# Kernel tuning notes

Measured on AMD Instinct MI355X. Metric: run time of the kernel, lower is better.

The kernel has to match this reference:

```python
import jax, jax.numpy as jnp
import numpy as np

BLOCK_SIZE = 256

def setup_inputs() -> dict:
    key = jax.random.key(0)
    k1, k2, k3 = jax.random.split(key, 3)
    B, H, S, D = 2, 16, 2048, 128
    return {
        "query": jax.random.normal(k1, (B, H, S, D), dtype=jnp.float32),
        "key": jax.random.normal(k2, (B, H, S, D), dtype=jnp.float32),
        "value": jax.random.normal(k3, (B, H, S, D), dtype=jnp.float32),
    }

def reference(query, key, value):
    # Faithful translation of the (non-flash) blocked attention:
    # for each query block i and key block j, a FULL softmax is taken over
    # just that key block, and the per-block outputs are summed over j.
    B, H, S, D = query.shape
    bs = min(BLOCK_SIZE, S)
    nb = S // bs  # S chosen to be a multiple of block_size
    scale = D ** -0.5
    q = query.reshape(B, H, nb, bs, D)
    k = key.reshape(B, H, nb, bs, D)
    v = value.reshape(B, H, nb, bs, D)
    # scores: [B,H,nb_q,nb_k,bs_q,bs_k]
    scores = jnp.einsum('bhiqd,bhjkd->bhijqk', q, k) * scale
    # per key-block softmax (over last axis only, NOT global online softmax)
    w = jax.nn.softmax(scores, axis=-1)
    # weighted values, summed over key blocks j (matches output += block_output)
    out = jnp.einsum('bhijqk,bhjkd->bhiqd', w, v)
    return out.reshape(B, H, S, D)
```

## Files before the change

kernel.cpp:

```cpp
#include <hip/hip_runtime.h>
#include <stdint.h>

#define S_LEN 2048
#define D_DIM 128

typedef __attribute__((ext_vector_type(8)))  short bf16x8;
typedef __attribute__((ext_vector_type(4)))  short bf16x4;
typedef __attribute__((ext_vector_type(4)))  float f32x4;
typedef __attribute__((ext_vector_type(2)))  float f32x2;
typedef __attribute__((ext_vector_type(16))) float f32x16;

__device__ __forceinline__ short f2bf(float f) {
  union { float f; uint32_t u; } c; c.f = f;
  uint32_t u = c.u;
  u += 0x7fffu + ((u >> 16) & 1u);
  return (short)(u >> 16);
}
__device__ __forceinline__ uint32_t pk2bf(float a, float b) {
#if __has_builtin(__builtin_amdgcn_cvt_pk_bf16_f32)
  typedef __attribute__((ext_vector_type(2))) __bf16 bf2;
  union { bf2 v; uint32_t u; } cv;
  cv.v = __builtin_amdgcn_cvt_pk_bf16_f32(a, b);
  return cv.u;
#else
  return (uint32_t)(uint16_t)f2bf(a) | (((uint32_t)(uint16_t)f2bf(b)) << 16);
#endif
}
__device__ __forceinline__ bf16x8 mk8(uint32_t a, uint32_t b, uint32_t c, uint32_t d) {
  union { uint32_t u[4]; bf16x8 v; } x;
  x.u[0] = a; x.u[1] = b; x.u[2] = c; x.u[3] = d;
  return x.v;
}
__device__ __forceinline__ void gl_lds16(const short* g, short* l) {
  __builtin_amdgcn_global_load_lds((const __attribute__((address_space(1))) void*)g,
                                   (__attribute__((address_space(3))) void*)l, 16, 0, 0);
}

__global__ __launch_bounds__(256) void pre_kernel(
    const float* __restrict__ K, const float* __restrict__ V,
    short* __restrict__ Kb, short* __restrict__ Vt) {
  const int t = threadIdx.x;
  if (blockIdx.x < 2048) {
    int i0 = blockIdx.x * 256 + t;
#pragma unroll
    for (int r = 0; r < 4; ++r) {
      int i = i0 + r * 524288;
      f32x4 v = ((const f32x4*)K)[i];
      *(uint2*)(Kb + (size_t)i * 4) = make_uint2(pk2bf(v[0], v[1]), pk2bf(v[2], v[3]));
    }
    return;
  }
  __shared__ __align__(16) short sTt[128 * 128];
  const int vb = blockIdx.x - 2048;
  const int bh = vb >> 4;
  const int k0 = (vb & 15) * 128;
  const float* src = V + ((size_t)bh * S_LEN + k0) * D_DIM;
#pragma unroll
  for (int i = 0; i < 16; ++i) {
    int e = i * 1024 + t * 4;
    int k = e >> 7, d4 = e & 127;
    f32x4 v = *(const f32x4*)(src + e);
#pragma unroll
    for (int jj = 0; jj < 4; ++jj) {
      int d = d4 + jj;
      sTt[d * 128 + (((k >> 3) ^ (d & 15)) << 3) + (k & 7)] = f2bf(v[jj]);
    }
  }
  __syncthreads();
  const int d = t >> 1;
  const int ph = (t & 1) * 64;
  short* out = Vt + ((size_t)bh * D_DIM + d) * S_LEN + k0 + ph;
#pragma unroll
  for (int g = 0; g < 8; ++g) {
    int pb = ph + g * 8;
    int B = pb >> 4;
    int rlo = pb & 15;
    int kb1 = B * 16 + (rlo ? 4 : 0);
    int kb2 = kb1 + 8;
    bf16x4 lo = *(const bf16x4*)&sTt[d * 128 + (((kb1 >> 3) ^ (d & 15)) << 3) + (kb1 & 7)];
    bf16x4 hi = *(const bf16x4*)&sTt[d * 128 + (((kb2 >> 3) ^ (d & 15)) << 3) + (kb2 & 7)];
    union { bf16x4 h[2]; bf16x8 v; } o;
    o.h[0] = lo; o.h[1] = hi;
    *(bf16x8*)(out + g * 8) = o.v;
  }
}

__global__ __launch_bounds__(256, 2) void attn_main(
    const short* __restrict__ Kb, const short* __restrict__ Vt,
    const float* __restrict__ Q, float* __restrict__ O) {
  __shared__ __align__(16) short ring[2][16384];
  __shared__ __align__(16) short sP[4096];
  __shared__ float sRed[128];
  __shared__ float sLinv[64];

  const int t = threadIdx.x;
  const int w = t >> 6;
  const int lane = t & 63;
  const int l31 = lane & 31;
  const int hi = lane >> 5;
  const int h = w & 1;
  const int qp = w >> 1;

  const int b = blockIdx.x;
  const int bh = (b & 7) * 4 + ((b >> 3) & 3);
  const int q0 = (b >> 5) * 64;

  const short* Kh = Kb + (size_t)bh * S_LEN * D_DIM;
  const short* Vh = Vt + (size_t)bh * D_DIM * S_LEN;

  const int kKey = t >> 4;
  const int kG   = (t & 15) ^ (kKey & 15);
  const int vD   = t >> 3;
  const int vG   = (t & 7) ^ (vD & 7);

  auto stageK = [&](int key0, int slot) {
    const short* src = Kh + (size_t)(key0 + kKey) * D_DIM + kG * 8;
    short* dst = &ring[slot][t * 8];
#pragma unroll
    for (int r = 0; r < 4; ++r) gl_lds16(src + r * 16 * D_DIM, dst + r * 2048);
  };
  auto stageV = [&](int key0, int slot) {
    const short* src = Vh + (size_t)vD * S_LEN + key0 + vG * 8;
    short* dst = &ring[slot][8192 + t * 8];
#pragma unroll
    for (int r = 0; r < 4; ++r) gl_lds16(src + (size_t)r * 32 * S_LEN, dst + r * 2048);
  };

  bf16x8 qf[8];
  {
    const float QSCALE = 0.12751743f;
    const float* Qg = Q + ((size_t)bh * S_LEN + q0 + qp * 32 + l31) * D_DIM;
#pragma unroll
    for (int ks = 0; ks < 8; ++ks) {
      f32x4 a = *(const f32x4*)(Qg + ks * 16 + hi * 8);
      f32x4 c = *(const f32x4*)(Qg + ks * 16 + hi * 8 + 4);
      qf[ks] = mk8(pk2bf(a[0] * QSCALE, a[1] * QSCALE), pk2bf(a[2] * QSCALE, a[3] * QSCALE),
                   pk2bf(c[0] * QSCALE, c[1] * QSCALE), pk2bf(c[2] * QSCALE, c[3] * QSCALE));
    }
  }

  int aK[8];
#pragma unroll
  for (int ks = 0; ks < 8; ++ks)
    aK[ks] = (h * 32 + l31) * 128 + (((2 * ks + hi) ^ (l31 & 15)) << 3);
  int aV[4];
#pragma unroll
  for (int u = 0; u < 4; ++u)
    aV[u] = (h * 64 + l31) * 64 + (((u * 2 + hi) ^ (l31 & 7)) << 3);

  f32x16 oa[2], oj[2];
#pragma unroll
  for (int d = 0; d < 2; ++d)
#pragma unroll
    for (int r = 0; r < 16; ++r) { oa[d][r] = 0.f; oj[d][r] = 0.f; }

  float ssum = 0.f;
  const int spOwn = ((qp * 2 + h) * 2) * 512 + lane * 8;

  stageK(0, 0); stageV(0, 0);

  for (int j = 0; j < 8; ++j) {
#pragma unroll
    for (int c = 0; c < 4; ++c) {
      const int G = j * 4 + c;
      const int slot = G & 1;
      __syncthreads();
      if (G + 1 < 32) { stageK((G + 1) * 64, slot ^ 1); stageV((G + 1) * 64, slot ^ 1); }

      if (c == 0 && j > 0) {
        f32x4 lv[4];
#pragma unroll
        for (int g = 0; g < 4; ++g) lv[g] = *(const f32x4*)&sLinv[qp * 32 + g * 8 + hi * 4];
#pragma unroll
        for (int d = 0; d < 2; ++d)
#pragma unroll
          for (int r = 0; r < 16; ++r) {
            oa[d][r] += oj[d][r] * lv[r >> 2][r & 3];
            oj[d][r] = 0.f;
          }
      }

      const short* pK = &ring[slot][0];
      f32x16 sc;
#pragma unroll
      for (int r = 0; r < 16; ++r) sc[r] = 0.f;
#pragma unroll
      for (int ks = 0; ks < 8; ++ks) {
        bf16x8 a = *(const bf16x8*)(pK + aK[ks]);
        sc = __builtin_amdgcn_mfma_f32_32x32x16_bf16(a, qf[ks], sc, 0, 0, 0);
      }
#pragma unroll
      for (int r = 0; r < 16; ++r) sc[r] = exp2f(sc[r]);
      float ps = 0.f;
#pragma unroll
      for (int r = 0; r < 16; ++r) ps += sc[r];
      ssum += ps;

      bf16x8 pf[2];
#pragma unroll
      for (int t2 = 0; t2 < 2; ++t2) {
        pf[t2] = mk8(pk2bf(sc[8 * t2 + 0], sc[8 * t2 + 1]), pk2bf(sc[8 * t2 + 2], sc[8 * t2 + 3]),
                     pk2bf(sc[8 * t2 + 4], sc[8 * t2 + 5]), pk2bf(sc[8 * t2 + 6], sc[8 * t2 + 7]));
        *(bf16x8*)(sP + spOwn + t2 * 512) = pf[t2];
      }
      if (c == 3) {
        ssum += __shfl_xor(ssum, 32);
        if (lane < 32) sRed[(qp * 32 + l31) * 2 + h] = ssum;
        ssum = 0.f;
      }
      __syncthreads();
      if (c == 3 && h == 0 && lane < 32) {
        f32x2 s2 = *(const f32x2*)&sRed[(qp * 32 + l31) * 2];
        sLinv[qp * 32 + l31] = __fdividef(1.0f, s2[0] + s2[1]);
      }

      const short* pV = &ring[slot][8192];
#pragma unroll
      for (int hw = 0; hw < 2; ++hw)
#pragma unroll
        for (int t2 = 0; t2 < 2; ++t2) {
          bf16x8 a = (hw == h) ? pf[t2]
                               : *(const bf16x8*)(sP + ((qp * 2 + hw) * 2 + t2) * 512 + lane * 8);
#pragma unroll
          for (int dt = 0; dt < 2; ++dt) {
            bf16x8 bv = *(const bf16x8*)(pV + aV[hw * 2 + t2] + dt * 2048);
            oj[dt] = __builtin_amdgcn_mfma_f32_32x32x16_bf16(a, bv, oj[dt], 0, 0, 0);
          }
        }
    }
  }

  __syncthreads();
  {
    f32x4 lv[4];
#pragma unroll
    for (int g = 0; g < 4; ++g) lv[g] = *(const f32x4*)&sLinv[qp * 32 + g * 8 + hi * 4];
    float* Og = O + ((size_t)bh * S_LEN + q0) * D_DIM;
#pragma unroll
    for (int d = 0; d < 2; ++d)
#pragma unroll
      for (int r = 0; r < 16; ++r) {
        float val = oa[d][r] + oj[d][r] * lv[r >> 2][r & 3];
        int row = qp * 32 + (r & 3) + 8 * (r >> 2) + 4 * hi;
        int col = h * 64 + d * 32 + l31;
        Og[row * D_DIM + col] = val;
      }
  }
}

extern "C" void kernel_launch(void* const* d_in, const int* in_sizes, int n_in,
                              void* d_out, int out_size, void* d_ws, size_t ws_size,
                              hipStream_t stream) {
  const float* Q = (const float*)d_in[0];
  const float* K = (const float*)d_in[1];
  const float* V = (const float*)d_in[2];
  float* Out = (float*)d_out;
  const size_t tElems = (size_t)32 * S_LEN * D_DIM;

  short* Kb  = (short*)d_ws;
  short* Vtb = Kb + tElems;

  pre_kernel<<<2560, 256, 0, stream>>>(K, V, Kb, Vtb);
  attn_main<<<1024, 256, 0, stream>>>(Kb, Vtb, Q, Out);
}
```

Before: 240.1 us.

## Split PV by key halves per wave, drop P LDS exchange, register-transpose V

The attention kernel now has each wave multiply its own P fragment against all 128 head dimensions, using the key half it computed scores for. This removes the shared-memory P exchange and one barrier per chunk. The two waves' partial outputs are summed through LDS once at the end. The V pre-pass transposes in registers with 16-bit packing instead of through LDS, and the K conversion uses fewer, larger blocks. The trade is that the output accumulators double to 128 floats per lane, which raises register pressure at two blocks per SM.

```diff
diff --git a/kernel.cpp b/kernel.cpp
--- a/kernel.cpp
+++ b/kernel.cpp
@@ -31,6 +31,12 @@
   x.u[0] = a; x.u[1] = b; x.u[2] = c; x.u[3] = d;
   return x.v;
 }
+__device__ __forceinline__ uint32_t lo16(uint32_t a, uint32_t b) {
+  return (a & 0xffffu) | (b << 16);
+}
+__device__ __forceinline__ uint32_t hi16(uint32_t a, uint32_t b) {
+  return (a >> 16) | (b & 0xffff0000u);
+}
 __device__ __forceinline__ void gl_lds16(const short* g, short* l) {
   __builtin_amdgcn_global_load_lds((const __attribute__((address_space(1))) void*)g,
                                    (__attribute__((address_space(3))) void*)l, 16, 0, 0);
@@ -40,48 +46,49 @@
     const float* __restrict__ K, const float* __restrict__ V,
     short* __restrict__ Kb, short* __restrict__ Vt) {
   const int t = threadIdx.x;
-  if (blockIdx.x < 2048) {
-    int i0 = blockIdx.x * 256 + t;
-#pragma unroll
-    for (int r = 0; r < 4; ++r) {
-      int i = i0 + r * 524288;
-      f32x4 v = ((const f32x4*)K)[i];
-      *(uint2*)(Kb + (size_t)i * 4) = make_uint2(pk2bf(v[0], v[1]), pk2bf(v[2], v[3]));
+  const int b = blockIdx.x;
+  if (b < 512) {
+    const f32x4* src = (const f32x4*)K + (size_t)b * 4096;
+    uint2* dst = (uint2*)Kb + (size_t)b * 4096;
+#pragma unroll
+    for (int it = 0; it < 16; ++it) {
+      f32x4 v = src[it * 256 + t];
+      dst[it * 256 + t] = make_uint2(pk2bf(v[0], v[1]), pk2bf(v[2], v[3]));
     }
     return;
   }
-  __shared__ __align__(16) short sTt[128 * 128];
-  const int vb = blockIdx.x - 2048;
+  const int vb = b - 512;
   const int bh = vb >> 4;
   const int k0 = (vb & 15) * 128;
   const float* src = V + ((size_t)bh * S_LEN + k0) * D_DIM;
-#pragma unroll
-  for (int i = 0; i < 16; ++i) {
-    int e = i * 1024 + t * 4;
-    int k = e >> 7, d4 = e & 127;
-    f32x4 v = *(const f32x4*)(src + e);
-#pragma unroll
-    for (int jj = 0; jj < 4; ++jj) {
-      int d = d4 + jj;
-      sTt[d * 128 + (((k >> 3) ^ (d & 15)) << 3) + (k & 7)] = f2bf(v[jj]);
-    }
-  }
-  __syncthreads();
-  const int d = t >> 1;
-  const int ph = (t & 1) * 64;
-  short* out = Vt + ((size_t)bh * D_DIM + d) * S_LEN + k0 + ph;
-#pragma unroll
-  for (int g = 0; g < 8; ++g) {
-    int pb = ph + g * 8;
-    int B = pb >> 4;
-    int rlo = pb & 15;
-    int kb1 = B * 16 + (rlo ? 4 : 0);
-    int kb2 = kb1 + 8;
-    bf16x4 lo = *(const bf16x4*)&sTt[d * 128 + (((kb1 >> 3) ^ (d & 15)) << 3) + (kb1 & 7)];
-    bf16x4 hi = *(const bf16x4*)&sTt[d * 128 + (((kb2 >> 3) ^ (d & 15)) << 3) + (kb2 & 7)];
-    union { bf16x4 h[2]; bf16x8 v; } o;
-    o.h[0] = lo; o.h[1] = hi;
-    *(bf16x8*)(out + g * 8) = o.v;
+  short* dstBase = Vt + (size_t)bh * D_DIM * S_LEN + k0;
+  const int dg = t & 31;
+#pragma unroll
+  for (int half = 0; half < 2; ++half) {
+    const int kg = (t >> 5) + half * 8;
+    uint32_t r[8][2];
+#pragma unroll
+    for (int rr = 0; rr < 8; ++rr) {
+      f32x4 v = *(const f32x4*)(src + (size_t)(kg * 8 + rr) * D_DIM + dg * 4);
+      r[rr][0] = pk2bf(v[0], v[1]);
+      r[rr][1] = pk2bf(v[2], v[3]);
+    }
+    const int base1 = (kg >> 1) * 16 + (kg & 1) * 4;
+#pragma unroll
+    for (int dd = 0; dd < 4; ++dd) {
+      const int wsel = dd >> 1;
+      uint32_t w0, w1, w2, w3;
+      if ((dd & 1) == 0) {
+        w0 = lo16(r[0][wsel], r[1][wsel]); w1 = lo16(r[2][wsel], r[3][wsel]);
+        w2 = lo16(r[4][wsel], r[5][wsel]); w3 = lo16(r[6][wsel], r[7][wsel]);
+      } else {
+        w0 = hi16(r[0][wsel], r[1][wsel]); w1 = hi16(r[2][wsel], r[3][wsel]);
+        w2 = hi16(r[4][wsel], r[5][wsel]); w3 = hi16(r[6][wsel], r[7][wsel]);
+      }
+      short* orow = dstBase + (size_t)(dg * 4 + dd) * S_LEN;
+      *(uint2*)(orow + base1)     = make_uint2(w0, w1);
+      *(uint2*)(orow + base1 + 8) = make_uint2(w2, w3);
+    }
   }
 }
 
@@ -89,7 +96,6 @@
     const short* __restrict__ Kb, const short* __restrict__ Vt,
     const float* __restrict__ Q, float* __restrict__ O) {
   __shared__ __align__(16) short ring[2][16384];
-  __shared__ __align__(16) short sP[4096];
   __shared__ float sRed[128];
   __shared__ float sLinv[64];
 
@@ -143,19 +149,18 @@
 #pragma unroll
   for (int ks = 0; ks < 8; ++ks)
     aK[ks] = (h * 32 + l31) * 128 + (((2 * ks + hi) ^ (l31 & 15)) << 3);
-  int aV[4];
-#pragma unroll
-  for (int u = 0; u < 4; ++u)
-    aV[u] = (h * 64 + l31) * 64 + (((u * 2 + hi) ^ (l31 & 7)) << 3);
-
-  f32x16 oa[2], oj[2];
-#pragma unroll
-  for (int d = 0; d < 2; ++d)
+  int aV2[2];
+#pragma unroll
+  for (int t2 = 0; t2 < 2; ++t2)
+    aV2[t2] = l31 * 64 + ((((h * 2 + t2) * 2 + hi) ^ (l31 & 7)) << 3);
+
+  f32x16 oa[4], oj[4];
+#pragma unroll
+  for (int d = 0; d < 4; ++d)
 #pragma unroll
     for (int r = 0; r < 16; ++r) { oa[d][r] = 0.f; oj[d][r] = 0.f; }
 
   float ssum = 0.f;
-  const int spOwn = ((qp * 2 + h) * 2) * 512 + lane * 8;
 
   stageK(0, 0); stageV(0, 0);
 
@@ -172,7 +177,7 @@
 #pragma unroll
         for (int g = 0; g < 4; ++g) lv[g] = *(const f32x4*)&sLinv[qp * 32 + g * 8 + hi * 4];
 #pragma unroll
-        for (int d = 0; d < 2; ++d)
+        for (int d = 0; d < 4; ++d)
 #pragma unroll
           for (int r = 0; r < 16; ++r) {
             oa[d][r] += oj[d][r] * lv[r >> 2][r & 3];
@@ -181,16 +186,21 @@
       }
 
       const short* pK = &ring[slot][0];
-      f32x16 sc;
-#pragma unroll
-      for (int r = 0; r < 16; ++r) sc[r] = 0.f;
-#pragma unroll
-      for (int ks = 0; ks < 8; ++ks) {
+      f32x16 sc, sc2;
+#pragma unroll
+      for (int r = 0; r < 16; ++r) { sc[r] = 0.f; sc2[r] = 0.f; }
+#pragma unroll
+      for (int ks = 0; ks < 4; ++ks) {
         bf16x8 a = *(const bf16x8*)(pK + aK[ks]);
         sc = __builtin_amdgcn_mfma_f32_32x32x16_bf16(a, qf[ks], sc, 0, 0, 0);
       }
 #pragma unroll
-      for (int r = 0; r < 16; ++r) sc[r] = exp2f(sc[r]);
+      for (int ks = 4; ks < 8; ++ks) {
+        bf16x8 a = *(const bf16x8*)(pK + aK[ks]);
+        sc2 = __builtin_amdgcn_mfma_f32_32x32x16_bf16(a, qf[ks], sc2, 0, 0, 0);
+      }
+#pragma unroll
+      for (int r = 0; r < 16; ++r) sc[r] = exp2f(sc[r] + sc2[r]);
       float ps = 0.f;
 #pragma unroll
       for (int r = 0; r < 16; ++r) ps += sc[r];
@@ -198,52 +208,63 @@
 
       bf16x8 pf[2];
 #pragma unroll
-      for (int t2 = 0; t2 < 2; ++t2) {
+      for (int t2 = 0; t2 < 2; ++t2)
         pf[t2] = mk8(pk2bf(sc[8 * t2 + 0], sc[8 * t2 + 1]), pk2bf(sc[8 * t2 + 2], sc[8 * t2 + 3]),
                      pk2bf(sc[8 * t2 + 4], sc[8 * t2 + 5]), pk2bf(sc[8 * t2 + 6], sc[8 * t2 + 7]));
-        *(bf16x8*)(sP + spOwn + t2 * 512) = pf[t2];
-      }
+
       if (c == 3) {
         ssum += __shfl_xor(ssum, 32);
         if (lane < 32) sRed[(qp * 32 + l31) * 2 + h] = ssum;
         ssum = 0.f;
-      }
-      __syncthreads();
-      if (c == 3 && h == 0 && lane < 32) {
-        f32x2 s2 = *(const f32x2*)&sRed[(qp * 32 + l31) * 2];
-        sLinv[qp * 32 + l31] = __fdividef(1.0f, s2[0] + s2[1]);
+        __syncthreads();
+        if (h == 0 && lane < 32) {
+          f32x2 s2 = *(const f32x2*)&sRed[(qp * 32 + l31) * 2];
+          sLinv[qp * 32 + l31] = __fdividef(1.0f, s2[0] + s2[1]);
+        }
       }
 
       const short* pV = &ring[slot][8192];
 #pragma unroll
-      for (int hw = 0; hw < 2; ++hw)
-#pragma unroll
-        for (int t2 = 0; t2 < 2; ++t2) {
-          bf16x8 a = (hw == h) ? pf[t2]
-                               : *(const bf16x8*)(sP + ((qp * 2 + hw) * 2 + t2) * 512 + lane * 8);
-#pragma unroll
-          for (int dt = 0; dt < 2; ++dt) {
-            bf16x8 bv = *(const bf16x8*)(pV + aV[hw * 2 + t2] + dt * 2048);
-            oj[dt] = __builtin_amdgcn_mfma_f32_32x32x16_bf16(a, bv, oj[dt], 0, 0, 0);
-          }
+      for (int t2 = 0; t2 < 2; ++t2) {
+#pragma unroll
+        for (int dt = 0; dt < 4; ++dt) {
+          bf16x8 bv = *(const bf16x8*)(pV + aV2[t2] + dt * 2048);
+          oj[dt] = __builtin_amdgcn_mfma_f32_32x32x16_bf16(pf[t2], bv, oj[dt], 0, 0, 0);
         }
+      }
     }
   }
 
   __syncthreads();
-  {
-    f32x4 lv[4];
-#pragma unroll
-    for (int g = 0; g < 4; ++g) lv[g] = *(const f32x4*)&sLinv[qp * 32 + g * 8 + hi * 4];
-    float* Og = O + ((size_t)bh * S_LEN + q0) * D_DIM;
-#pragma unroll
-    for (int d = 0; d < 2; ++d)
+  f32x4 lv[4];
+#pragma unroll
+  for (int g = 0; g < 4; ++g) lv[g] = *(const f32x4*)&sLinv[qp * 32 + g * 8 + hi * 4];
+  float of[4][16];
+#pragma unroll
+  for (int d = 0; d < 4; ++d)
+#pragma unroll
+    for (int r = 0; r < 16; ++r) of[d][r] = oa[d][r] + oj[d][r] * lv[r >> 2][r & 3];
+
+  float* ex = (float*)&ring[0][0];
+  if (h == 1) {
+#pragma unroll
+    for (int d = 0; d < 4; ++d)
 #pragma unroll
       for (int r = 0; r < 16; ++r) {
-        float val = oa[d][r] + oj[d][r] * lv[r >> 2][r & 3];
-        int row = qp * 32 + (r & 3) + 8 * (r >> 2) + 4 * hi;
-        int col = h * 64 + d * 32 + l31;
-        Og[row * D_DIM + col] = val;
+        int q = (r & 3) + 8 * (r >> 2) + 4 * hi;
+        ex[qp * 4096 + q * 128 + d * 32 + l31] = of[d][r];
+      }
+  }
+  __syncthreads();
+  if (h == 0) {
+    float* Og = O + ((size_t)bh * S_LEN + q0 + qp * 32) * D_DIM;
+#pragma unroll
+    for (int d = 0; d < 4; ++d)
+#pragma unroll
+      for (int r = 0; r < 16; ++r) {
+        int q = (r & 3) + 8 * (r >> 2) + 4 * hi;
+        float val = of[d][r] + ex[qp * 4096 + q * 128 + d * 32 + l31];
+        Og[(size_t)q * D_DIM + d * 32 + l31] = val;
       }
   }
 }
@@ -260,6 +281,6 @@
   short* Kb  = (short*)d_ws;
   short* Vtb = Kb + tElems;
 
-  pre_kernel<<<2560, 256, 0, stream>>>(K, V, Kb, Vtb);
+  pre_kernel<<<1024, 256, 0, stream>>>(K, V, Kb, Vtb);
   attn_main<<<1024, 256, 0, stream>>>(Kb, Vtb, Q, Out);
 }
```

New measurement: 269.4 us. 1.12x slower.
